# Optimization experiments

Measured on AMD Instinct MI355X. Metric: run time of the kernel, lower is better.

Reference implementation:

```python
import jax, jax.numpy as jnp
import numpy as np

TAU = 2.0        # spikingjelly LIFNode default tau
VTH = 1.0        # v_threshold
ALPHA = 2.0      # ATan surrogate default alpha
NWIN = (4, 4, 4)
TOPK = 4
HEADS = 8

@jax.custom_vjp
def spike(x):
    return (x >= 0.0).astype(x.dtype)

def _spike_fwd(x):
    return spike(x), x

def _spike_bwd(x, g):
    # ATan surrogate: d/dx ~ alpha/2 / (1 + (pi/2 * alpha * x)^2)
    s = (jnp.pi / 2) * ALPHA * x
    return (g * (ALPHA / 2) / (1 + s * s),)

spike.defvjp(_spike_fwd, _spike_bwd)

def lif(x):
    # fresh-state single-step LIF: H = x/tau, spike if H >= v_threshold
    return spike(x / TAU - VTH)

def setup_inputs() -> dict:
    key = jax.random.key(0)
    ks = jax.random.split(key, 4)
    T, B, Lt, Lh, Lw, C = 4, 2, 8, 32, 32, 256
    x = jax.random.normal(ks[0], (T, B, Lt, Lh, Lw, C), jnp.float32)
    W_qkv = jax.random.normal(ks[1], (C, 3 * C), jnp.float32) / np.sqrt(C)
    b_qkv = jnp.zeros((3 * C,), jnp.float32)
    W_proj = jax.random.normal(ks[2], (C, C), jnp.float32) / np.sqrt(C)
    b_proj = jnp.zeros((C,), jnp.float32)
    return {"x": x, "W_qkv": W_qkv, "b_qkv": b_qkv, "W_proj": W_proj, "b_proj": b_proj}

def reference(x, W_qkv, b_qkv, W_proj, b_proj):
    T, B, Lt, Lh, Lw, C = x.shape
    wt, wh, ww = NWIN
    H = HEADS
    hd = C // H
    nw = wt * wh * ww
    pt, ph, pw = Lt // wt, Lh // wh, Lw // ww
    ws = pt * ph * pw

    # windowize: [T,B,nw,ws,C]
    xw = x.reshape(T, B, wt, pt, wh, ph, ww, pw, C)
    xw = xw.transpose(0, 1, 2, 4, 6, 3, 5, 7, 8).reshape(T, B, nw, ws, C)

    # region-level routing scores over windows
    region = xw.sum(0).mean(2)                                  # [B,nw,C]
    scores = jnp.einsum('bic,bjc->bij', region, region) * (hd ** -0.5)
    idx = jax.lax.top_k(scores, TOPK)[1]                        # [B,nw,topk]

    qkv = xw @ W_qkv + b_qkv                                    # [T,B,nw,ws,3C]
    q, k, v = jnp.split(qkv, 3, axis=-1)
    q, k, v = lif(q), lif(k), lif(v)
    q = q.reshape(T, B, nw, ws, H, hd)
    k = k.reshape(T, B, nw, ws, H, hd)
    v = v.reshape(T, B, nw, ws, H, hd)

    # per-batch gather of topk routed windows' k/v
    gather = jax.vmap(lambda kb, ib: kb[:, ib], in_axes=(1, 0), out_axes=1)
    k_g = gather(k, idx).reshape(T, B, nw, TOPK * ws, H, hd)    # [T,B,nw,topk*ws,H,hd]
    v_g = gather(v, idx).reshape(T, B, nw, TOPK * ws, H, hd)

    # linear (kernelized) attention: kv = k^T v, out = q kv / (q sum_k)
    kv = jnp.einsum('tbnshd,tbnshe->tbnhde', k_g, v_g)          # [T,B,nw,H,hd,hd]
    out = jnp.einsum('tbnshd,tbnhde->tbnshe', q, kv)            # [T,B,nw,ws,H,hd]
    ksum = k_g.sum(3)                                           # [T,B,nw,H,hd]
    D = jnp.einsum('tbnshd,tbnhd->tbnsh', q, ksum)[..., None]   # [T,B,nw,ws,H,1]
    out = out / (D + 1e-6)

    out = out.reshape(T, B, nw, ws, C) @ W_proj + b_proj

    # un-windowize
    out = out.reshape(T, B, wt, wh, ww, pt, ph, pw, C)
    out = out.transpose(0, 1, 2, 5, 3, 6, 4, 7, 8).reshape(T, B, Lt, Lh, Lw, C)
    return out
```

## Files before the change

kernel.cpp:

```cpp
#include <hip/hip_runtime.h>
#include <cstdint>
#include <cstddef>

#define T_    4
#define B_    2
#define NW_   64
#define WS_   128
#define C_    256
#define NC3   768
#define H_    8
#define HD_   32
#define TOPK_ 4
#define RCAP  131072
#define BAND  0.008f
#define RBCAP 512

#define OFF_A2     0ull
#define OFF_BQ     67108864ull
#define OFF_BP     67502080ull
#define OFF_QM     67895296ull
#define OFF_KB     69992448ull
#define OFF_VB     72089600ull
#define OFF_KV     74186752ull
#define OFF_PART   91488256ull
#define OFF_REGION 92012544ull
#define OFF_IDX    92143616ull
#define OFF_RL     92145664ull
#define OFF_RC     92669952ull

typedef short short8 __attribute__((ext_vector_type(8)));
typedef float floatx4 __attribute__((ext_vector_type(4)));

__device__ __forceinline__ short f2bf(float f) {
    unsigned u = __float_as_uint(f);
    unsigned r = (u + 0x7fffu + ((u >> 16) & 1u)) >> 16;
    return (short)r;
}
__device__ __forceinline__ float bf2f(short h) {
    return __uint_as_float(((unsigned)(unsigned short)h) << 16);
}

__device__ __forceinline__ void gload_lds16(const void* g, void* l) {
    __builtin_amdgcn_global_load_lds(
        (const __attribute__((address_space(1))) unsigned*)g,
        (__attribute__((address_space(3))) unsigned*)l,
        16, 0, 0);
}

__device__ __forceinline__ int xoff_row(int g, int s) {
    int tb = g >> 6;
    int n  = g & 63;
    int iwt = n >> 4, iwh = (n >> 2) & 3, iww = n & 3;
    int ipt = s >> 6, iph = (s >> 3) & 7, ipw = s & 7;
    int lt = iwt * 2 + ipt, lh = iwh * 8 + iph, lw = iww * 8 + ipw;
    return (((tb * 8 + lt) * 32 + lh) * 32 + lw) * 256;
}

__global__ __launch_bounds__(256) void k_prep(const float* __restrict__ x,
        const float* __restrict__ Wqkv, const float* __restrict__ Wp,
        float* __restrict__ part, short* __restrict__ A2,
        short* __restrict__ Bq, short* __restrict__ Bp) {
    const int bid = blockIdx.x;
    const int tid = threadIdx.x;
    if (bid < 512) {
        int g = bid;
        int c = tid;
        const int ktAh = c >> 5, ktAl = 8 + (c >> 5);
        const int octsh = ((c >> 3) & 3) << 4, sub = c & 7;
        float acc = 0.f;
        for (int s = 0; s < WS_; ++s) {
            float v = x[xoff_row(g, s) + c];
            acc += v;
            short hi = f2bf(v);
            short lo = f2bf(v - bf2f(hi));
            int lane = (s & 15) | octsh;
            size_t base = ((size_t)(g * 8 + (s >> 4))) * 16;
            A2[(base + ktAh) * 512 + lane * 8 + sub] = hi;
            A2[(base + ktAl) * 512 + lane * 8 + sub] = lo;
        }
        part[g * C_ + c] = acc;
    } else if (bid < 1280) {
        int u = bid - 512;
        int ke = u & 255;
        int n = (u >> 8) * 256 + tid;
        float wv = Wqkv[(size_t)ke * NC3 + n];
        short o = f2bf(wv);
        int gj = n >> 4, lmn = n & 15, ktB = ke >> 5, oct = (ke >> 3) & 3, sub = ke & 7;
        Bq[(size_t)((gj * 8 + ktB) * 64 + (lmn | (oct << 4))) * 8 + sub] = o;
    } else {
        int ke = bid - 1280;
        int n = tid;
        float wv = Wp[(size_t)(ke & 255) * 256 + n];
        short hi = f2bf(wv);
        short o = (ke < 512) ? hi : f2bf(wv - bf2f(hi));
        int gj = n >> 4, lmn = n & 15, ktB = ke >> 5, oct = (ke >> 3) & 3, sub = ke & 7;
        Bp[(size_t)((gj * 24 + ktB) * 64 + (lmn | (oct << 4))) * 8 + sub] = o;
    }
}

__global__ __launch_bounds__(256) void k_region(const float* __restrict__ part,
                                                float* __restrict__ region) {
    int bn = blockIdx.x;
    int c = threadIdx.x;
    int b = bn >> 6, n = bn & 63;
    float acc = 0.f;
    for (int t = 0; t < T_; ++t) acc += part[((t * 2 + b) * 64 + n) * C_ + c];
    region[bn * C_ + c] = acc * (1.0f / 128.0f);
}

__global__ __launch_bounds__(64) void k_scores(const float* __restrict__ region,
                                               int* __restrict__ idx) {
    int bi = blockIdx.x;
    int b = bi >> 6, i = bi & 63;
    int tid = threadIdx.x;
    __shared__ float ri[C_];
    __shared__ float sc[64];
    for (int c = tid; c < C_; c += 64) ri[c] = region[(b * 64 + i) * C_ + c];
    __syncthreads();
    const float* rj = region + (size_t)(b * 64 + tid) * C_;
    float dot = 0.f;
    for (int c = 0; c < C_; ++c) dot += ri[c] * rj[c];
    sc[tid] = dot * 0.17677669529663687f;
    __syncthreads();
    if (tid == 0) {
        for (int kk = 0; kk < TOPK_; ++kk) {
            float best = -INFINITY; int bj = 0;
            for (int j = 0; j < 64; ++j)
                if (sc[j] > best) { best = sc[j]; bj = j; }
            idx[bi * TOPK_ + kk] = bj;
            sc[bj] = -INFINITY;
        }
    }
}

__device__ __forceinline__ unsigned p4(unsigned xv) {
    return (xv & 1u) | ((xv >> 7) & 2u) | ((xv >> 14) & 4u) | ((xv >> 21) & 8u);
}

__global__ __launch_bounds__(256, 2) void qkv_mfma(const short* __restrict__ A2,
        const short* __restrict__ Bq, const float* __restrict__ bias,
        unsigned* __restrict__ qm, unsigned* __restrict__ kb,
        unsigned* __restrict__ vb, unsigned* __restrict__ rl,
        unsigned* __restrict__ rcnt) {
    __shared__ __align__(16) char stg[2][32768];
    __shared__ unsigned rbuf[RBCAP];
    __shared__ unsigned lcnt, sbase;
    const int bid = blockIdx.x;
    const int x8 = bid & 7;
    const int y = bid >> 3;
    const int p = y % 3;
    const int mb = x8 + ((y / 3) << 3);
    const int tid = threadIdx.x;
    const int wv = tid >> 6, lane = tid & 63;
    const int wm = wv >> 1, wn = wv & 1;
    const int lm = lane & 15, lq = lane >> 4;

    if (tid == 0) lcnt = 0;

    const char* Ag = (const char*)(A2 + (size_t)mb * 65536);
    const char* Bg = (const char*)(Bq + (size_t)p * 65536);
    const int laneoff = lane * 16;

#define STAGE_CHUNK(buf, ktB_)                                                 \
    {                                                                          \
        _Pragma("unroll")                                                      \
        for (int k = 0; k < 4; ++k) {                                          \
            int slot = k * 4 + wv;                                             \
            int gi = slot >> 1, hl = slot & 1;                                 \
            const char* src = Ag + (((gi * 16) + (ktB_) + hl * 8) << 10) + laneoff; \
            gload_lds16(src, &stg[buf][k * 4096 + wv * 1024 + laneoff]);       \
        }                                                                      \
        _Pragma("unroll")                                                      \
        for (int k = 0; k < 4; ++k) {                                          \
            int slot = k * 4 + wv;                                             \
            const char* src = Bg + ((slot * 8 + (ktB_)) << 10) + laneoff;      \
            gload_lds16(src, &stg[buf][16384 + k * 4096 + wv * 1024 + laneoff]); \
        }                                                                      \
    }

    floatx4 acc[4][8];
#pragma unroll
    for (int i = 0; i < 4; ++i)
#pragma unroll
        for (int j = 0; j < 8; ++j) acc[i][j] = (floatx4)0.f;

    STAGE_CHUNK(0, 0);
    __syncthreads();

    for (int ktB = 0; ktB < 8; ++ktB) {
        int cur = ktB & 1;
        if (ktB < 7) STAGE_CHUNK(cur ^ 1, ktB + 1);
        const char* sb = &stg[cur][0];
        short8 ah[4], al[4], bf[8];
#pragma unroll
        for (int j = 0; j < 8; ++j)
            bf[j] = *(const short8*)(sb + 16384 + ((wn * 8 + j) << 10) + laneoff);
#pragma unroll
        for (int i = 0; i < 4; ++i) {
            ah[i] = *(const short8*)(sb + (((wm * 4 + i) * 2 + 0) << 10) + laneoff);
            al[i] = *(const short8*)(sb + (((wm * 4 + i) * 2 + 1) << 10) + laneoff);
        }
#pragma unroll
        for (int i = 0; i < 4; ++i)
#pragma unroll
            for (int j = 0; j < 8; ++j)
                acc[i][j] = __builtin_amdgcn_mfma_f32_16x16x32_bf16(
                    ah[i], bf[j], acc[i][j], 0, 0, 0);
#pragma unroll
        for (int i = 0; i < 4; ++i)
#pragma unroll
            for (int j = 0; j < 8; ++j)
                acc[i][j] = __builtin_amdgcn_mfma_f32_16x16x32_bf16(
                    al[i], bf[j], acc[i][j], 0, 0, 0);
        __syncthreads();
    }

    unsigned char* sp = (unsigned char*)&stg[0][0];
#pragma unroll
    for (int i = 0; i < 4; ++i) {
#pragma unroll
        for (int j = 0; j < 8; ++j) {
            int cb = wn * 128 + j * 16 + lm;
            int cg = p * 256 + cb;
            float bj = bias[cg];
#pragma unroll
            for (int r = 0; r < 4; ++r) {
                int s = wm * 64 + i * 16 + lq * 4 + r;
                float v = acc[i][j][r] + bj;
                if (fabsf(v - 2.0f) < BAND) {
                    unsigned ent = ((unsigned)mb << 17) | ((unsigned)s << 10) | (unsigned)cg;
                    unsigned slot = atomicAdd(&lcnt, 1u);
                    if (slot < RBCAP) {
                        rbuf[slot] = ent;
                    } else {
                        unsigned gs = atomicAdd(rcnt, 1u);
                        if (gs < RCAP) rl[gs] = ent;
                    }
                }
                sp[s * 264 + cb] = (v >= 2.0f) ? 1 : 0;
            }
        }
    }
    __syncthreads();

    unsigned cnt = lcnt;
    if (cnt > RBCAP) cnt = RBCAP;
    if (tid == 0) sbase = atomicAdd(rcnt, cnt);
    __syncthreads();
    for (unsigned e = tid; e < cnt; e += 256) {
        unsigned slot = sbase + e;
        if (slot < RCAP) rl[slot] = rbuf[e];
    }

    if (p == 0) {
        const unsigned* spw = (const unsigned*)sp;
#pragma unroll
        for (int t = 0; t < 4; ++t) {
            int w = t * 256 + tid;
            int s = w >> 3, h = w & 7;
            unsigned m = 0;
#pragma unroll
            for (int q = 0; q < 8; ++q)
                m |= p4(spw[s * 66 + h * 8 + q]) << (q * 4);
            qm[(size_t)mb * 1024 + w] = m;
        }
    } else {
        unsigned wrd[4];
#pragma unroll
        for (int w2 = 0; w2 < 4; ++w2) {
            unsigned m = 0;
#pragma unroll
            for (int ii = 0; ii < 32; ++ii)
                m |= (unsigned)(sp[(w2 * 32 + ii) * 264 + tid] & 1) << ii;
            wrd[w2] = m;
        }
        uint4 o; o.x = wrd[0]; o.y = wrd[1]; o.z = wrd[2]; o.w = wrd[3];
        *(uint4*)(((p == 1) ? kb : vb) + ((size_t)mb * 256 + tid) * 4) = o;
    }
}

__global__ __launch_bounds__(256) void rescue_fix(const float* __restrict__ x,
        const float* __restrict__ W, const float* __restrict__ bias,
        const unsigned* __restrict__ rl, const unsigned* __restrict__ rcnt,
        unsigned* __restrict__ qm, unsigned* __restrict__ kb,
        unsigned* __restrict__ vb) {
    unsigned n = *rcnt; if (n > RCAP) n = RCAP;
    unsigned gid = blockIdx.x * 256 + threadIdx.x;
    unsigned stride = gridDim.x * 256;
    for (unsigned e = gid; e < n; e += stride) {
        unsigned ent = rl[e];
        int mb = ent >> 17, s = (ent >> 10) & 127, cg = ent & 1023;
        const float* ar = x + xoff_row(mb, s);
        const float* wc = W + cg;
        float da = 0.f;
#pragma unroll 4
        for (int k4 = 0; k4 < 64; ++k4) {
            float4 a4 = *(const float4*)(ar + k4 * 4);
            da = fmaf(a4.x, wc[(size_t)(k4 * 4 + 0) * NC3], da);
            da = fmaf(a4.y, wc[(size_t)(k4 * 4 + 1) * NC3], da);
            da = fmaf(a4.z, wc[(size_t)(k4 * 4 + 2) * NC3], da);
            da = fmaf(a4.w, wc[(size_t)(k4 * 4 + 3) * NC3], da);
        }
        da += bias[cg];
        int spk = (da >= 2.0f) ? 1 : 0;
        if (cg < 256) {
            int h = cg >> 5, d = cg & 31;
            unsigned* wp = qm + (size_t)mb * 1024 + s * 8 + h;
            unsigned bit = 1u << d;
            int have = (*wp & bit) ? 1 : 0;
            if (have != spk) atomicXor(wp, bit);
        } else {
            unsigned* tgt = (cg < 512) ? kb : vb;
            int c = cg & 255;
            unsigned* wp = tgt + ((size_t)mb * 256 + c) * 4 + (s >> 5);
            unsigned bit = 1u << (s & 31);
            int have = (*wp & bit) ? 1 : 0;
            if (have != spk) atomicXor(wp, bit);
        }
    }
}

__global__ __launch_bounds__(256) void kv_bits(const unsigned* __restrict__ kb,
        const unsigned* __restrict__ vb, const int* __restrict__ idx,
        short* __restrict__ kvf) {
    int g = blockIdx.x;
    int tb = g >> 6, n = g & 63, b = tb & 1;
    int tid = threadIdx.x;
    __shared__ uint4 kbl[1024];
    __shared__ uint4 vbl[1024];
    __shared__ int widx[TOPK_];
    if (tid < TOPK_) widx[tid] = idx[(b * 64 + n) * TOPK_ + tid];
    __syncthreads();
#pragma unroll
    for (int kk = 0; kk < TOPK_; ++kk) {
        int g2 = tb * 64 + widx[kk];
        kbl[kk * 256 + tid] = *(const uint4*)&kb[((size_t)g2 * 256 + tid) * 4];
        vbl[kk * 256 + tid] = *(const uint4*)&vb[((size_t)g2 * 256 + tid) * 4];
    }
    __syncthreads();
    int h = tid >> 5, e = tid & 31;
    int ei = e >> 4;
    uint4 vw0 = vbl[0 * 256 + h * 32 + e];
    uint4 vw1 = vbl[1 * 256 + h * 32 + e];
    uint4 vw2 = vbl[2 * 256 + h * 32 + e];
    uint4 vw3 = vbl[3 * 256 + h * 32 + e];
#pragma unroll
    for (int oct = 0; oct < 4; ++oct) {
        short8 hi8, lo8;
#pragma unroll
        for (int dd = 0; dd < 8; ++dd) {
            int d = oct * 8 + dd;
            uint4 k0 = kbl[0 * 256 + h * 32 + d];
            uint4 k1 = kbl[1 * 256 + h * 32 + d];
            uint4 k2 = kbl[2 * 256 + h * 32 + d];
            uint4 k3 = kbl[3 * 256 + h * 32 + d];
            int acc = __popc(k0.x & vw0.x) + __popc(k0.y & vw0.y)
                    + __popc(k0.z & vw0.z) + __popc(k0.w & vw0.w)
                    + __popc(k1.x & vw1.x) + __popc(k1.y & vw1.y)
                    + __popc(k1.z & vw1.z) + __popc(k1.w & vw1.w)
                    + __popc(k2.x & vw2.x) + __popc(k2.y & vw2.y)
                    + __popc(k2.z & vw2.z) + __popc(k2.w & vw2.w)
                    + __popc(k3.x & vw3.x) + __popc(k3.y & vw3.y)
                    + __popc(k3.z & vw3.z) + __popc(k3.w & vw3.w);
            float v = (float)acc;
            short hv = f2bf(v);
            hi8[dd] = hv;
            lo8[dd] = f2bf(v - bf2f(hv));
        }
        int ln = (e & 15) | (oct << 4);
        *(short8*)&kvf[((((size_t)g * 8 + h) * 2 + 0) * 2 + ei) * 512 + ln * 8] = hi8;
        *(short8*)&kvf[((((size_t)g * 8 + h) * 2 + 1) * 2 + ei) * 512 + ln * 8] = lo8;
    }
}

__global__ __launch_bounds__(256) void attn_proj(const unsigned* __restrict__ qm,
        const short* __restrict__ kvf, const unsigned* __restrict__ kb,
        const int* __restrict__ idx, const short* __restrict__ Bp,
        const float* __restrict__ bias, float* __restrict__ out) {
    __shared__ __align__(16) short aw[16384];
    __shared__ unsigned qb[256];
    __shared__ float ksl[256];
    __shared__ float denl[256];
    __shared__ int widx[TOPK_];
    const int bid = blockIdx.x;
    const int g = bid >> 2, qr = bid & 3;
    const int tb = g >> 6, n = g & 63, b = tb & 1;
    const int tid = threadIdx.x;
    if (tid < TOPK_) widx[tid] = idx[(b * 64 + n) * TOPK_ + tid];
    __syncthreads();
    float ks = 0.f;
#pragma unroll
    for (int kk = 0; kk < TOPK_; ++kk) {
        uint4 kw = *(const uint4*)&kb[((size_t)(tb * 64 + widx[kk]) * 256 + tid) * 4];
        ks += (float)(__popc(kw.x) + __popc(kw.y) + __popc(kw.z) + __popc(kw.w));
    }
    ksl[tid] = ks;
    qb[tid] = qm[(size_t)g * 1024 + qr * 256 + tid];
    __syncthreads();

    {
        int h = tid >> 5, sl = tid & 31;
        unsigned qw = qb[sl * 8 + h];
        float den = 0.f;
#pragma unroll
        for (int d = 0; d < 32; ++d)
            den += ((qw >> d) & 1u) ? ksl[h * 32 + d] : 0.f;
        denl[tid] = den;
    }
    __syncthreads();

    const int wvw = tid >> 6, lane = tid & 63;
    const int oct = lane >> 4, l15 = lane & 15;

    floatx4 nacc[2][2][2];
#pragma unroll
    for (int h2 = 0; h2 < 2; ++h2)
#pragma unroll
        for (int mi = 0; mi < 2; ++mi)
#pragma unroll
            for (int ei = 0; ei < 2; ++ei) nacc[h2][mi][ei] = (floatx4)0.f;

#pragma unroll
    for (int h2 = 0; h2 < 2; ++h2) {
        int h = wvw * 2 + h2;
        short8 a0, a1;
        {
            unsigned byt = (qb[(l15)*8 + h] >> (oct * 8)) & 0xffu;
#pragma unroll
            for (int j = 0; j < 8; ++j)
                a0[j] = ((byt >> j) & 1u) ? (short)0x3F80 : (short)0;
        }
        {
            unsigned byt = (qb[(16 + l15)*8 + h] >> (oct * 8)) & 0xffu;
#pragma unroll
            for (int j = 0; j < 8; ++j)
                a1[j] = ((byt >> j) & 1u) ? (short)0x3F80 : (short)0;
        }
#pragma unroll
        for (int ei = 0; ei < 2; ++ei) {
            short8 bh = *(const short8*)&kvf[((((size_t)g * 8 + h) * 2 + 0) * 2 + ei) * 512 + lane * 8];
            short8 bl = *(const short8*)&kvf[((((size_t)g * 8 + h) * 2 + 1) * 2 + ei) * 512 + lane * 8];
            nacc[h2][0][ei] = __builtin_amdgcn_mfma_f32_16x16x32_bf16(a0, bh, nacc[h2][0][ei], 0, 0, 0);
            nacc[h2][0][ei] = __builtin_amdgcn_mfma_f32_16x16x32_bf16(a0, bl, nacc[h2][0][ei], 0, 0, 0);
            nacc[h2][1][ei] = __builtin_amdgcn_mfma_f32_16x16x32_bf16(a1, bh, nacc[h2][1][ei], 0, 0, 0);
            nacc[h2][1][ei] = __builtin_amdgcn_mfma_f32_16x16x32_bf16(a1, bl, nacc[h2][1][ei], 0, 0, 0);
        }
    }

#pragma unroll
    for (int h2 = 0; h2 < 2; ++h2) {
        int h = wvw * 2 + h2;
#pragma unroll
        for (int mi = 0; mi < 2; ++mi) {
#pragma unroll
            for (int ei = 0; ei < 2; ++ei) {
                int e = ei * 16 + l15;
                int lane2base = (((e >> 3) & 3) << 4);
                int sub = e & 7;
#pragma unroll
                for (int r = 0; r < 4; ++r) {
                    int sl = mi * 16 + oct * 4 + r;
                    float rv = nacc[h2][mi][ei][r] / (denl[h * 32 + sl] + 1e-6f);
                    short hi = f2bf(rv), lo = f2bf(rv - bf2f(hi));
                    int lane2 = (sl & 15) | lane2base;
                    aw[((mi * 16 + h) * 64 + lane2) * 8 + sub] = hi;
                    aw[((mi * 16 + 8 + h) * 64 + lane2) * 8 + sub] = lo;
                }
            }
        }
    }
    __syncthreads();

    const int lm = lane & 15, lq = lane >> 4;
    floatx4 pacc[2][4];
#pragma unroll
    for (int i = 0; i < 2; ++i)
#pragma unroll
        for (int j = 0; j < 4; ++j) pacc[i][j] = (floatx4)0.f;
    const short* Bb = Bp + ((size_t)(wvw * 4) * 24) * 512 + lane * 8;
#pragma unroll 2
    for (int kt = 0; kt < 24; ++kt) {
        int ktA = (kt < 16) ? kt : kt - 16;
        short8 af[2], bf[4];
#pragma unroll
        for (int i = 0; i < 2; ++i)
            af[i] = *(const short8*)&aw[((i * 16 + ktA) * 64 + lane) * 8];
#pragma unroll
        for (int j = 0; j < 4; ++j)
            bf[j] = *(const short8*)(Bb + (size_t)(j * 24 + kt) * 512);
#pragma unroll
        for (int i = 0; i < 2; ++i)
#pragma unroll
            for (int j = 0; j < 4; ++j)
                pacc[i][j] = __builtin_amdgcn_mfma_f32_16x16x32_bf16(
                    af[i], bf[j], pacc[i][j], 0, 0, 0);
    }
    __syncthreads();

    float* ow = (float*)aw;
#pragma unroll
    for (int i = 0; i < 2; ++i) {
#pragma unroll
        for (int j = 0; j < 4; ++j) {
            int c = wvw * 64 + j * 16 + lm;
            float bj = bias[c];
#pragma unroll
            for (int r = 0; r < 4; ++r)
                ow[(i * 16 + lq * 4 + r) * 256 + c] = pacc[i][j][r] + bj;
        }
    }
    __syncthreads();

    int sl2 = tid >> 3, pc = (tid & 7) * 32;
    int off = xoff_row(g, qr * 32 + sl2) + pc;
#pragma unroll
    for (int q = 0; q < 8; ++q)
        *(float4*)(out + off + q * 4) = *(const float4*)&ow[sl2 * 256 + pc + q * 4];
}

extern "C" void kernel_launch(void* const* d_in, const int* in_sizes, int n_in,
                              void* d_out, int out_size, void* d_ws, size_t ws_size,
                              hipStream_t stream) {
    (void)in_sizes; (void)n_in; (void)out_size; (void)ws_size;
    const float* x    = (const float*)d_in[0];
    const float* Wqkv = (const float*)d_in[1];
    const float* bqkv = (const float*)d_in[2];
    const float* Wp   = (const float*)d_in[3];
    const float* bp   = (const float*)d_in[4];
    char* ws = (char*)d_ws;
    short*    A2    = (short*)   (ws + OFF_A2);
    short*    Bq    = (short*)   (ws + OFF_BQ);
    short*    Bpj   = (short*)   (ws + OFF_BP);
    unsigned* qmv   = (unsigned*)(ws + OFF_QM);
    unsigned* kb    = (unsigned*)(ws + OFF_KB);
    unsigned* vb    = (unsigned*)(ws + OFF_VB);
    short*    kvf   = (short*)   (ws + OFF_KV);
    float*    part  = (float*)   (ws + OFF_PART);
    float*    region= (float*)   (ws + OFF_REGION);
    int*      idxb  = (int*)     (ws + OFF_IDX);
    unsigned* rl    = (unsigned*)(ws + OFF_RL);
    unsigned* rcnt  = (unsigned*)(ws + OFF_RC);
    float*    out   = (float*)d_out;

    hipMemsetAsync(rcnt, 0, 4, stream);
    k_prep     <<<2048, 256, 0, stream>>>(x, Wqkv, Wp, part, A2, Bq, Bpj);
    k_region   <<<128, 256, 0, stream>>>(part, region);
    k_scores   <<<128,  64, 0, stream>>>(region, idxb);
    qkv_mfma   <<<1536, 256, 0, stream>>>(A2, Bq, bqkv, qmv, kb, vb, rl, rcnt);
    rescue_fix <<<256, 256, 0, stream>>>(x, Wqkv, bqkv, rl, rcnt, qmv, kb, vb);
    kv_bits    <<<512, 256, 0, stream>>>(kb, vb, idxb, kvf);
    attn_proj  <<<2048, 256, 0, stream>>>(qmv, kvf, kb, idxb, Bpj, bp, out);
}
```

Baseline: 217.1 us.

## Vectorize A2 packing in prep and fuse routing into the rescue kernel

The prep kernel's x-to-bf16 split loop is rewritten so each lane loads float4 pairs and writes short8 vectors straight into the MFMA fragment layout, instead of scalar strided stores. The window partial sums are reduced through a 64 KB shared buffer. The separate region and score/top-k kernels are removed, and that work runs in two extra blocks appended to the rescue kernel, which saves two launches. The risks are the large shared-memory footprint in both kernels, which cuts occupancy, and a serialized per-batch top-k running in only two blocks.

```diff
diff --git a/kernel.cpp b/kernel.cpp
--- a/kernel.cpp
+++ b/kernel.cpp
@@ -23,7 +23,6 @@
 #define OFF_VB     72089600ull
 #define OFF_KV     74186752ull
 #define OFF_PART   91488256ull
-#define OFF_REGION 92012544ull
 #define OFF_IDX    92143616ull
 #define OFF_RL     92145664ull
 #define OFF_RC     92669952ull
@@ -60,25 +59,50 @@
         const float* __restrict__ Wqkv, const float* __restrict__ Wp,
         float* __restrict__ part, short* __restrict__ A2,
         short* __restrict__ Bq, short* __restrict__ Bp) {
+    __shared__ float psum[256][64];
     const int bid = blockIdx.x;
     const int tid = threadIdx.x;
     if (bid < 512) {
         int g = bid;
+        int w = tid >> 6, L = tid & 63;
+        int l15 = L & 15, oq = L >> 4;
+        float acc[64];
+#pragma unroll
+        for (int q = 0; q < 64; ++q) acc[q] = 0.f;
+        for (int sb2 = 0; sb2 < 2; ++sb2) {
+            int sblk = w * 2 + sb2;
+            int s = sblk * 16 + l15;
+            const float* xr = x + xoff_row(g, s);
+            size_t rowb = ((size_t)(g * 8 + sblk)) * 16;
+#pragma unroll
+            for (int kt = 0; kt < 8; ++kt) {
+                int c0 = kt * 32 + oq * 8;
+                float4 v0 = *(const float4*)(xr + c0);
+                float4 v1 = *(const float4*)(xr + c0 + 4);
+                float vv[8] = {v0.x, v0.y, v0.z, v0.w, v1.x, v1.y, v1.z, v1.w};
+                short8 hi, lo;
+#pragma unroll
+                for (int j = 0; j < 8; ++j) {
+                    acc[kt * 8 + j] += vv[j];
+                    short h = f2bf(vv[j]);
+                    hi[j] = h;
+                    lo[j] = f2bf(vv[j] - bf2f(h));
+                }
+                *(short8*)&A2[(rowb + kt) * 512 + (size_t)L * 8] = hi;
+                *(short8*)&A2[(rowb + 8 + kt) * 512 + (size_t)L * 8] = lo;
+            }
+        }
+#pragma unroll
+        for (int q = 0; q < 64; ++q) psum[tid][q] = acc[q];
+        __syncthreads();
         int c = tid;
-        const int ktAh = c >> 5, ktAl = 8 + (c >> 5);
-        const int octsh = ((c >> 3) & 3) << 4, sub = c & 7;
-        float acc = 0.f;
-        for (int s = 0; s < WS_; ++s) {
-            float v = x[xoff_row(g, s) + c];
-            acc += v;
-            short hi = f2bf(v);
-            short lo = f2bf(v - bf2f(hi));
-            int lane = (s & 15) | octsh;
-            size_t base = ((size_t)(g * 8 + (s >> 4))) * 16;
-            A2[(base + ktAh) * 512 + lane * 8 + sub] = hi;
-            A2[(base + ktAl) * 512 + lane * 8 + sub] = lo;
-        }
-        part[g * C_ + c] = acc;
+        int ktc = c >> 5, oqc = (c >> 3) & 3, jc = c & 7;
+        float tot = 0.f;
+        for (int ww = 0; ww < 4; ++ww)
+#pragma unroll
+            for (int l = 0; l < 16; ++l)
+                tot += psum[ww * 64 + oqc * 16 + l][ktc * 8 + jc];
+        part[g * C_ + c] = tot;
     } else if (bid < 1280) {
         int u = bid - 512;
         int ke = u & 255;
@@ -95,41 +119,6 @@
         short o = (ke < 512) ? hi : f2bf(wv - bf2f(hi));
         int gj = n >> 4, lmn = n & 15, ktB = ke >> 5, oct = (ke >> 3) & 3, sub = ke & 7;
         Bp[(size_t)((gj * 24 + ktB) * 64 + (lmn | (oct << 4))) * 8 + sub] = o;
-    }
-}
-
-__global__ __launch_bounds__(256) void k_region(const float* __restrict__ part,
-                                                float* __restrict__ region) {
-    int bn = blockIdx.x;
-    int c = threadIdx.x;
-    int b = bn >> 6, n = bn & 63;
-    float acc = 0.f;
-    for (int t = 0; t < T_; ++t) acc += part[((t * 2 + b) * 64 + n) * C_ + c];
-    region[bn * C_ + c] = acc * (1.0f / 128.0f);
-}
-
-__global__ __launch_bounds__(64) void k_scores(const float* __restrict__ region,
-                                               int* __restrict__ idx) {
-    int bi = blockIdx.x;
-    int b = bi >> 6, i = bi & 63;
-    int tid = threadIdx.x;
-    __shared__ float ri[C_];
-    __shared__ float sc[64];
-    for (int c = tid; c < C_; c += 64) ri[c] = region[(b * 64 + i) * C_ + c];
-    __syncthreads();
-    const float* rj = region + (size_t)(b * 64 + tid) * C_;
-    float dot = 0.f;
-    for (int c = 0; c < C_; ++c) dot += ri[c] * rj[c];
-    sc[tid] = dot * 0.17677669529663687f;
-    __syncthreads();
-    if (tid == 0) {
-        for (int kk = 0; kk < TOPK_; ++kk) {
-            float best = -INFINITY; int bj = 0;
-            for (int j = 0; j < 64; ++j)
-                if (sc[j] > best) { best = sc[j]; bj = j; }
-            idx[bi * TOPK_ + kk] = bj;
-            sc[bj] = -INFINITY;
-        }
     }
 }
 
@@ -279,15 +268,48 @@
     }
 }
 
-__global__ __launch_bounds__(256) void rescue_fix(const float* __restrict__ x,
+__global__ __launch_bounds__(256) void rescue_rs(const float* __restrict__ x,
         const float* __restrict__ W, const float* __restrict__ bias,
         const unsigned* __restrict__ rl, const unsigned* __restrict__ rcnt,
         unsigned* __restrict__ qm, unsigned* __restrict__ kb,
-        unsigned* __restrict__ vb) {
+        unsigned* __restrict__ vb, const float* __restrict__ part,
+        int* __restrict__ idx) {
+    __shared__ float reg[64][256];
+    __shared__ float sc2[64][64];
+    const int bid = blockIdx.x;
+    const int tid = threadIdx.x;
+    if (bid >= 256) {
+        int b = bid - 256;
+        for (int n = 0; n < 64; ++n) {
+            float a = 0.f;
+#pragma unroll
+            for (int t = 0; t < 4; ++t)
+                a += part[((t * 2 + b) * 64 + n) * C_ + tid];
+            reg[n][tid] = a * (1.0f / 128.0f);
+        }
+        __syncthreads();
+        for (int k = 0; k < 16; ++k) {
+            int id = tid * 16 + k;
+            int i = id >> 6, j = id & 63;
+            float dot = 0.f;
+            for (int c = 0; c < C_; ++c) dot += reg[i][c] * reg[j][c];
+            sc2[i][j] = dot * 0.17677669529663687f;
+        }
+        __syncthreads();
+        if (tid < 64) {
+            for (int kk = 0; kk < TOPK_; ++kk) {
+                float best = -INFINITY; int bj = 0;
+                for (int j = 0; j < 64; ++j)
+                    if (sc2[tid][j] > best) { best = sc2[tid][j]; bj = j; }
+                idx[(b * 64 + tid) * TOPK_ + kk] = bj;
+                sc2[tid][bj] = -INFINITY;
+            }
+        }
+        return;
+    }
     unsigned n = *rcnt; if (n > RCAP) n = RCAP;
-    unsigned gid = blockIdx.x * 256 + threadIdx.x;
-    unsigned stride = gridDim.x * 256;
-    for (unsigned e = gid; e < n; e += stride) {
+    unsigned gid = bid * 256 + tid;
+    for (unsigned e = gid; e < n; e += 65536u) {
         unsigned ent = rl[e];
         int mb = ent >> 17, s = (ent >> 10) & 127, cg = ent & 1023;
         const float* ar = x + xoff_row(mb, s);
@@ -536,7 +558,6 @@
     unsigned* vb    = (unsigned*)(ws + OFF_VB);
     short*    kvf   = (short*)   (ws + OFF_KV);
     float*    part  = (float*)   (ws + OFF_PART);
-    float*    region= (float*)   (ws + OFF_REGION);
     int*      idxb  = (int*)     (ws + OFF_IDX);
     unsigned* rl    = (unsigned*)(ws + OFF_RL);
     unsigned* rcnt  = (unsigned*)(ws + OFF_RC);
@@ -544,10 +565,8 @@
 
     hipMemsetAsync(rcnt, 0, 4, stream);
     k_prep     <<<2048, 256, 0, stream>>>(x, Wqkv, Wp, part, A2, Bq, Bpj);
-    k_region   <<<128, 256, 0, stream>>>(part, region);
-    k_scores   <<<128,  64, 0, stream>>>(region, idxb);
     qkv_mfma   <<<1536, 256, 0, stream>>>(A2, Bq, bqkv, qmv, kb, vb, rl, rcnt);
-    rescue_fix <<<256, 256, 0, stream>>>(x, Wqkv, bqkv, rl, rcnt, qmv, kb, vb);
+    rescue_rs  <<<258, 256, 0, stream>>>(x, Wqkv, bqkv, rl, rcnt, qmv, kb, vb, part, idxb);
     kv_bits    <<<512, 256, 0, stream>>>(kb, vb, idxb, kvf);
     attn_proj  <<<2048, 256, 0, stream>>>(qmv, kvf, kb, idxb, Bpj, bp, out);
 }
```

Result: slower. 256.2 us (+18.0%).
